# Kernel tuning notes

Hardware: AMD Instinct MI355X
Metric: run time of the kernel (lower is better)

## Reference

```python
import jax, jax.numpy as jnp
import numpy as np
import math

B, H, S, D = 2, 16, 2048, 64

def setup_inputs() -> dict:
    key = jax.random.key(0)
    kq, kk, kv, km = jax.random.split(key, 4)
    return {
        "query": jax.random.normal(kq, (B, H, S, D), dtype=jnp.float32),
        "key": jax.random.normal(kk, (B, H, S, D), dtype=jnp.float32),
        "value": jax.random.normal(kv, (B, H, S, D), dtype=jnp.float32),
        "mask": jax.random.randint(km, (B, 1, S, S), 0, 2, dtype=jnp.int32),
    }

def reference(query, key, value, mask):
    d = query.shape[-1]
    # scores: [B, H, S, S]
    scores = jnp.einsum("bhqd,bhkd->bhqk", query, key) / math.sqrt(d)
    masking_value = -1e9 if scores.dtype == jnp.float32 else -1e4
    scores = jnp.where(mask == 0, jnp.asarray(masking_value, scores.dtype), scores)
    p_attn = jax.nn.softmax(scores, axis=-1)
    out = jnp.einsum("bhqk,bhkd->bhqd", p_attn, value)
    return (out, p_attn)
```

## Files before the change

kernel.cpp:

```cpp
#include <hip/hip_runtime.h>

#define B_ 2
#define H_ 16
#define S_ 2048
#define D_ 64

typedef short v8s __attribute__((ext_vector_type(8)));
typedef float v4f __attribute__((ext_vector_type(4)));
typedef unsigned short u16;
typedef unsigned int   u32;
typedef unsigned long long u64;

__device__ __forceinline__ u32 pk2(float a, float b) {
    u32 ua = __float_as_uint(a) + 0x8000u;
    u32 ub = __float_as_uint(b) + 0x8000u;
    return __builtin_amdgcn_perm(ub, ua, 0x07060302u);
}

__device__ __forceinline__ v8s cvt8(const float* __restrict__ p, float s) {
    float4 x = ((const float4*)p)[0];
    float4 y = ((const float4*)p)[1];
    union { u32 u[4]; v8s v; } r;
    r.u[0] = pk2(x.x * s, x.y * s);
    r.u[1] = pk2(x.z * s, x.w * s);
    r.u[2] = pk2(y.x * s, y.y * s);
    r.u[3] = pk2(y.z * s, y.w * s);
    return r.v;
}

__device__ __forceinline__ void gll16(const void* g, void* l) {
    __builtin_amdgcn_global_load_lds(
        (const __attribute__((address_space(1))) u32*)g,
        (__attribute__((address_space(3))) u32*)l, 16, 0, 0);
}


__global__ void cvt_bf16_k(const float* __restrict__ src, u16* __restrict__ dst) {
    size_t i = (size_t)blockIdx.x * blockDim.x + threadIdx.x;
    const float* p = src + i * 8;
    float4 a = ((const float4*)p)[0], b = ((const float4*)p)[1];
    uint4 o;
    o.x = pk2(a.x, a.y); o.y = pk2(a.z, a.w);
    o.z = pk2(b.x, b.y); o.w = pk2(b.z, b.w);
    ((uint4*)dst)[i] = o;
}

__global__ void vtrans_k(const float* __restrict__ V, u16* __restrict__ Vt) {
    __shared__ u16 t[64][66];
    const int bh = blockIdx.y, s0 = blockIdx.x * 64;
    const int tid = threadIdx.x;
    {
        const int r = tid >> 2, c0 = (tid & 3) * 16;
        const float* p = V + ((size_t)bh * S_ + s0 + r) * D_ + c0;
        float4 f0 = ((const float4*)p)[0], f1 = ((const float4*)p)[1];
        float4 f2 = ((const float4*)p)[2], f3 = ((const float4*)p)[3];
        u32* tw = (u32*)&t[r][c0];
        tw[0] = pk2(f0.x, f0.y); tw[1] = pk2(f0.z, f0.w);
        tw[2] = pk2(f1.x, f1.y); tw[3] = pk2(f1.z, f1.w);
        tw[4] = pk2(f2.x, f2.y); tw[5] = pk2(f2.z, f2.w);
        tw[6] = pk2(f3.x, f3.y); tw[7] = pk2(f3.z, f3.w);
    }
    __syncthreads();
    {
        const int d = tid >> 2, t2 = tid & 3;
        const int G = t2 >> 1, hh = t2 & 1;
        const int e0 = G * 32 + hh * 8;
        u32 o[8];
        #pragma unroll
        for (int u = 0; u < 8; ++u)
            o[u] = (u32)t[e0 + u][d] | ((u32)t[e0 + 16 + u][d] << 16);
        u16* q = Vt + ((size_t)bh * D_ + d) * S_ + s0 + G * 32 + hh * 16;
        ((uint4*)q)[0] = make_uint4(o[0], o[1], o[2], o[3]);
        ((uint4*)q)[1] = make_uint4(o[4], o[5], o[6], o[7]);
    }
}

__global__ void mbits_k(const int* __restrict__ mask, u64* __restrict__ mb) {
    size_t i = (size_t)blockIdx.x * blockDim.x + threadIdx.x;
    u64 bal = __ballot(mask[i] != 0);
    if ((threadIdx.x & 63) == 0) mb[i >> 6] = bal;
}

__global__ __launch_bounds__(256, 4)
void attn_fast(const float* __restrict__ Q, const u16* __restrict__ Kb,
               const u16* __restrict__ Vt, const u32* __restrict__ mbits,
               float* __restrict__ out, float* __restrict__ P)
{
    __shared__ __align__(16) char LS[32768];

    const int tid = threadIdx.x;
    const int w = tid >> 6, lane = tid & 63;
    const int n = lane & 15, g = lane >> 4;

    const int x = blockIdx.x;
    const int xcd = x & 7, kk = x >> 3;
    const int bh = xcd * 4 + (kk >> 5);
    const int qb = kk & 31;
    const int b = bh >> 4;
    const int q0 = qb * 64 + w * 16;

    const float* qrow = Q + ((size_t)bh * S_ + q0 + n) * D_;
    const v8s aq0 = cvt8(qrow + g * 8, 0.125f);
    const v8s aq1 = cvt8(qrow + 32 + g * 8, 0.125f);

    const int srow = 16 * w + (lane >> 3);
    const int swz16 = (((lane & 7) ^ (srow & 7)) << 4);
    const char* kB  = (const char*)(Kb + (size_t)bh * S_ * D_) + (size_t)srow * 128 + swz16;
    const char* vB  = (const char*)(Vt + (size_t)bh * D_ * S_) + (size_t)srow * 4096 + swz16;
    const char* kBA = (const char*)(Kb + (size_t)bh * S_ * D_)
                      + (size_t)(32 * w + (lane >> 3)) * 128 + swz16;

    const int C = n * 128 + (((g) ^ (n & 7)) << 4);

    const u32* mroww = mbits + ((size_t)b * S_ + q0 + n) * 64;

    float sum = 0.f;
    {
        #pragma unroll
        for (int c = 0; c < 4; ++c)
            gll16(kBA + c * 1024, LS + (size_t)w * 4096 + c * 1024);
        uint4 mnx = *(const uint4*)(mroww);
        __syncthreads();

        for (int T = 0; T < 16; ++T) {
            const char* KA = LS + (T & 1) * 16384;
            if (T < 15) {
                const char* src = kBA + (size_t)(T + 1) * 16384;
                char* dst = LS + ((T + 1) & 1) * 16384 + (size_t)w * 4096;
                #pragma unroll
                for (int c = 0; c < 4; ++c) gll16(src + c * 1024, dst + c * 1024);
            }
            uint4 mc = mnx;
            if (T < 15) mnx = *(const uint4*)(mroww + (T + 1) * 4);

            v4f acc[8];
            __builtin_amdgcn_s_setprio(1);
            #pragma unroll
            for (int s = 0; s < 8; ++s) {
                v8s kf0 = *(const v8s*)(KA + s * 2048 + C);
                v8s kf1 = *(const v8s*)(KA + s * 2048 + (C ^ 64));
                v4f z = {0.f, 0.f, 0.f, 0.f};
                z = __builtin_amdgcn_mfma_f32_16x16x32_bf16(kf0, aq0, z, 0, 0, 0);
                acc[s] = __builtin_amdgcn_mfma_f32_16x16x32_bf16(kf1, aq1, z, 0, 0, 0);
            }
            __builtin_amdgcn_s_setprio(0);
            float ps0 = 0.f, ps1 = 0.f;
            #pragma unroll
            for (int s = 0; s < 8; ++s) {
                u32 wrd = (s >> 1) == 0 ? mc.x : (s >> 1) == 1 ? mc.y
                        : (s >> 1) == 2 ? mc.z : mc.w;
                #pragma unroll
                for (int i = 0; i < 4; ++i) {
                    float e = ((wrd >> ((s & 1) * 16 + 4 * g + i)) & 1)
                              ? __expf(acc[s][i]) : 0.f;
                    if (s & 1) ps1 += e; else ps0 += e;
                }
            }
            sum += ps0 + ps1;
            __syncthreads();
        }
    }
    sum += __shfl_xor(sum, 16, 64);
    sum += __shfl_xor(sum, 32, 64);
    const float inv = 1.0f / sum;

    float* pbB = P + ((size_t)bh * S_ + q0 + n) * S_;
    v4f o0 = {0.f, 0.f, 0.f, 0.f}, o1 = o0, o2 = o0, o3 = o0;
    {
        #pragma unroll
        for (int c = 0; c < 2; ++c) {
            gll16(kB + (size_t)c * 1024,  LS + (size_t)w * 2048 + c * 1024);
            gll16(vB + (size_t)c * 32768, LS + 8192 + (size_t)w * 2048 + c * 1024);
        }
        uint2 mnx = *(const uint2*)(mroww);
        __syncthreads();

        for (int t = 0; t < 32; ++t) {
            const char* Kc = LS + (t & 1) * 16384;
            const char* Vc = Kc + 8192;
            if (t < 31) {
                char* dstb = LS + ((t + 1) & 1) * 16384;
                const char* ks = kB + (size_t)(t + 1) * 8192;
                const char* vs = vB + (size_t)(t + 1) * 128;
                #pragma unroll
                for (int c = 0; c < 2; ++c) {
                    gll16(ks + (size_t)c * 1024,  dstb + (size_t)w * 2048 + c * 1024);
                    gll16(vs + (size_t)c * 32768, dstb + 8192 + (size_t)w * 2048 + c * 1024);
                }
            }
            uint2 mc = mnx;
            if (t < 31) mnx = *(const uint2*)(mroww + (t + 1) * 2);

            v4f a[4];
            __builtin_amdgcn_s_setprio(1);
            #pragma unroll
            for (int s = 0; s < 4; ++s) {
                v8s kf0 = *(const v8s*)(Kc + s * 2048 + C);
                v8s kf1 = *(const v8s*)(Kc + s * 2048 + (C ^ 64));
                v4f z = {0.f, 0.f, 0.f, 0.f};
                z = __builtin_amdgcn_mfma_f32_16x16x32_bf16(kf0, aq0, z, 0, 0, 0);
                a[s] = __builtin_amdgcn_mfma_f32_16x16x32_bf16(kf1, aq1, z, 0, 0, 0);
            }
            __builtin_amdgcn_s_setprio(0);

            float* pt = pbB + (size_t)t * 64;
            #pragma unroll
            for (int kg = 0; kg < 2; ++kg) {
                u32 wrd = kg ? mc.y : mc.x;
                v4f p0, p1;
                #pragma unroll
                for (int i = 0; i < 4; ++i) {
                    p0[i] = ((wrd >> (4 * g + i)) & 1)
                            ? __expf(a[2 * kg][i]) * inv : 0.f;
                    p1[i] = ((wrd >> (16 + 4 * g + i)) & 1)
                            ? __expf(a[2 * kg + 1][i]) * inv : 0.f;
                }
                __builtin_nontemporal_store(p0, (v4f*)(pt + kg * 32 + 4 * g));
                __builtin_nontemporal_store(p1, (v4f*)(pt + kg * 32 + 16 + 4 * g));
                union { u32 u[4]; v8s v; } ap;
                #pragma unroll
                for (int i = 0; i < 4; ++i) ap.u[i] = pk2(p0[i], p1[i]);
                __builtin_amdgcn_s_setprio(1);
                v8s vf0 = *(const v8s*)(Vc + 0 * 2048 + (C ^ (kg << 6)));
                v8s vf1 = *(const v8s*)(Vc + 1 * 2048 + (C ^ (kg << 6)));
                v8s vf2 = *(const v8s*)(Vc + 2 * 2048 + (C ^ (kg << 6)));
                v8s vf3 = *(const v8s*)(Vc + 3 * 2048 + (C ^ (kg << 6)));
                o0 = __builtin_amdgcn_mfma_f32_16x16x32_bf16(ap.v, vf0, o0, 0, 0, 0);
                o1 = __builtin_amdgcn_mfma_f32_16x16x32_bf16(ap.v, vf1, o1, 0, 0, 0);
                o2 = __builtin_amdgcn_mfma_f32_16x16x32_bf16(ap.v, vf2, o2, 0, 0, 0);
                o3 = __builtin_amdgcn_mfma_f32_16x16x32_bf16(ap.v, vf3, o3, 0, 0, 0);
                __builtin_amdgcn_s_setprio(0);
            }
            __syncthreads();
        }
    }

    float* obase = out + ((size_t)bh * S_ + q0 + 4 * g) * D_ + n;
    #pragma unroll
    for (int i = 0; i < 4; ++i) {
        __builtin_nontemporal_store(o0[i], obase + (size_t)i * D_);
        __builtin_nontemporal_store(o1[i], obase + (size_t)i * D_ + 16);
        __builtin_nontemporal_store(o2[i], obase + (size_t)i * D_ + 32);
        __builtin_nontemporal_store(o3[i], obase + (size_t)i * D_ + 48);
    }
}

__global__ __launch_bounds__(256, 4)
void attn_fb(const float* __restrict__ Q, const float* __restrict__ K,
             const float* __restrict__ V, const int* __restrict__ mask,
             float* __restrict__ out, float* __restrict__ P)
{
    __shared__ u16 ldsbuf[4][640];
    const int tid = threadIdx.x;
    const int w = tid >> 6, lane = tid & 63;
    const int n = lane & 15, g = lane >> 4;
    const int qb = blockIdx.x, h = blockIdx.y, b = blockIdx.z;
    const int bh = b * H_ + h;
    const int q0 = qb * 64 + w * 16;

    const float* qrow = Q + ((size_t)bh * S_ + q0 + n) * D_;
    const v8s aq0 = cvt8(qrow + g * 8, 0.125f);
    const v8s aq1 = cvt8(qrow + 32 + g * 8, 0.125f);

    const int* mrow = mask + ((size_t)b * S_ + q0 + g * 4) * S_ + n;
    const float* kfbase = K + ((size_t)bh * S_ + n) * D_ + g * 8;

    auto loadK = [&](int key0, int dh) -> v8s {
        return cvt8(kfbase + (size_t)key0 * D_ + dh * 32, 1.0f);
    };
    auto loadM = [&](int i, int k0) -> u32 {
        u32 r = 0;
        if (mrow[(size_t)i * S_ + k0]) r |= 1u << n;
        if (mrow[(size_t)i * S_ + k0 + 16]) r |= 1u << (n + 16);
        return r;
    };
    auto loadV = [&](int k0, int dt) -> v8s {
        union { u32 u[4]; v8s v; } r;
        const float* vp = V + ((size_t)bh * S_ + k0 + g * 4) * D_ + dt * 16 + n;
        #pragma unroll
        for (int p2 = 0; p2 < 4; ++p2) {
            float fa = vp[(size_t)p2 * D_];
            float fb = vp[(size_t)(16 + p2) * D_];
            r.u[p2] = pk2(fa, fb);
        }
        return r.v;
    };

    v4f sum = {0.f, 0.f, 0.f, 0.f};
    for (int k0 = 0; k0 < S_; k0 += 32) {
        v4f a0 = {0.f, 0.f, 0.f, 0.f}, a1 = {0.f, 0.f, 0.f, 0.f};
        a0 = __builtin_amdgcn_mfma_f32_16x16x32_bf16(aq0, loadK(k0, 0), a0, 0, 0, 0);
        a0 = __builtin_amdgcn_mfma_f32_16x16x32_bf16(aq1, loadK(k0, 1), a0, 0, 0, 0);
        a1 = __builtin_amdgcn_mfma_f32_16x16x32_bf16(aq0, loadK(k0 + 16, 0), a1, 0, 0, 0);
        a1 = __builtin_amdgcn_mfma_f32_16x16x32_bf16(aq1, loadK(k0 + 16, 1), a1, 0, 0, 0);
        #pragma unroll
        for (int i = 0; i < 4; ++i) {
            u32 mw = loadM(i, k0);
            float e0 = ((mw >> n) & 1) ? __expf(a0[i]) : 0.f;
            float e1 = ((mw >> (n + 16)) & 1) ? __expf(a1[i]) : 0.f;
            sum[i] += e0 + e1;
        }
    }
    #pragma unroll
    for (int i = 0; i < 4; ++i) {
        float s = sum[i];
        s += __shfl_xor(s, 1, 64);
        s += __shfl_xor(s, 2, 64);
        s += __shfl_xor(s, 4, 64);
        s += __shfl_xor(s, 8, 64);
        sum[i] = 1.0f / s;
    }

    char* ldsw = (char*)&ldsbuf[w][0];
    float* pbase = P + ((size_t)bh * S_ + q0 + g * 4) * S_ + n;
    v4f o0 = {0.f, 0.f, 0.f, 0.f}, o1 = o0, o2 = o0, o3 = o0;

    for (int k0 = 0; k0 < S_; k0 += 32) {
        v4f a0 = {0.f, 0.f, 0.f, 0.f}, a1 = {0.f, 0.f, 0.f, 0.f};
        a0 = __builtin_amdgcn_mfma_f32_16x16x32_bf16(aq0, loadK(k0, 0), a0, 0, 0, 0);
        a0 = __builtin_amdgcn_mfma_f32_16x16x32_bf16(aq1, loadK(k0, 1), a0, 0, 0, 0);
        a1 = __builtin_amdgcn_mfma_f32_16x16x32_bf16(aq0, loadK(k0 + 16, 0), a1, 0, 0, 0);
        a1 = __builtin_amdgcn_mfma_f32_16x16x32_bf16(aq1, loadK(k0 + 16, 1), a1, 0, 0, 0);
        #pragma unroll
        for (int i = 0; i < 4; ++i) {
            u32 mw = loadM(i, k0);
            float p0 = ((mw >> n) & 1) ? __expf(a0[i]) * sum[i] : 0.f;
            float p1 = ((mw >> (n + 16)) & 1) ? __expf(a1[i]) * sum[i] : 0.f;
            pbase[(size_t)i * S_ + k0] = p0;
            pbase[(size_t)i * S_ + k0 + 16] = p1;
            *(u32*)(ldsw + (g * 4 + i) * 80 + (n >> 2) * 16 + (n & 3) * 4) = pk2(p0, p1);
        }
        v8s ap = *(const v8s*)(ldsw + n * 80 + g * 16);
        o0 = __builtin_amdgcn_mfma_f32_16x16x32_bf16(ap, loadV(k0, 0), o0, 0, 0, 0);
        o1 = __builtin_amdgcn_mfma_f32_16x16x32_bf16(ap, loadV(k0, 1), o1, 0, 0, 0);
        o2 = __builtin_amdgcn_mfma_f32_16x16x32_bf16(ap, loadV(k0, 2), o2, 0, 0, 0);
        o3 = __builtin_amdgcn_mfma_f32_16x16x32_bf16(ap, loadV(k0, 3), o3, 0, 0, 0);
    }

    float* obase = out + ((size_t)bh * S_ + q0 + g * 4) * D_ + n;
    #pragma unroll
    for (int i = 0; i < 4; ++i) {
        obase[(size_t)i * D_]      = o0[i];
        obase[(size_t)i * D_ + 16] = o1[i];
        obase[(size_t)i * D_ + 32] = o2[i];
        obase[(size_t)i * D_ + 48] = o3[i];
    }
}

extern "C" void kernel_launch(void* const* d_in, const int* in_sizes, int n_in,
                              void* d_out, int out_size, void* d_ws, size_t ws_size,
                              hipStream_t stream)
{
    (void)in_sizes; (void)n_in; (void)out_size;
    const float* Q = (const float*)d_in[0];
    const float* K = (const float*)d_in[1];
    const float* V = (const float*)d_in[2];
    const int* mask = (const int*)d_in[3];
    float* out = (float*)d_out;
    float* P = out + (size_t)B_ * H_ * S_ * D_;

    const size_t kb_b = (size_t)B_ * H_ * S_ * D_ * 2;
    const size_t vt_b = kb_b;
    const size_t mb_b = (size_t)B_ * S_ * S_ / 8;

    if (ws_size >= kb_b + vt_b + mb_b) {
        u16* Kb = (u16*)d_ws;
        u16* Vt = (u16*)((char*)d_ws + kb_b);
        u64* mb = (u64*)((char*)d_ws + kb_b + vt_b);
        cvt_bf16_k<<<(B_ * H_ * S_ * D_) / (256 * 8), 256, 0, stream>>>(K, Kb);
        vtrans_k<<<dim3(S_ / 64, B_ * H_), 256, 0, stream>>>(V, Vt);
        mbits_k<<<(B_ * S_ * S_) / 256, 256, 0, stream>>>(mask, mb);
        attn_fast<<<B_ * H_ * (S_ / 64), 256, 0, stream>>>(Q, Kb, Vt, (const u32*)mb, out, P);
    } else {
        attn_fb<<<dim3(S_ / 64, H_, B_), 256, 0, stream>>>(Q, K, V, mask, out, P);
    }
}
```

Before: 687.5 us.

## Load K/V MFMA fragments directly from global memory into registers, dropping LDS staging

```diff
diff --git a/kernel.cpp b/kernel.cpp
--- a/kernel.cpp
+++ b/kernel.cpp
@@ -26,12 +26,6 @@
     r.u[2] = pk2(y.x * s, y.y * s);
     r.u[3] = pk2(y.z * s, y.w * s);
     return r.v;
-}
-
-__device__ __forceinline__ void gll16(const void* g, void* l) {
-    __builtin_amdgcn_global_load_lds(
-        (const __attribute__((address_space(1))) u32*)g,
-        (__attribute__((address_space(3))) u32*)l, 16, 0, 0);
 }
 
 
@@ -86,8 +80,6 @@
                const u16* __restrict__ Vt, const u32* __restrict__ mbits,
                float* __restrict__ out, float* __restrict__ P)
 {
-    __shared__ __align__(16) char LS[32768];
-
     const int tid = threadIdx.x;
     const int w = tid >> 6, lane = tid & 63;
     const int n = lane & 15, g = lane >> 4;
@@ -103,62 +95,54 @@
     const v8s aq0 = cvt8(qrow + g * 8, 0.125f);
     const v8s aq1 = cvt8(qrow + 32 + g * 8, 0.125f);
 
-    const int srow = 16 * w + (lane >> 3);
-    const int swz16 = (((lane & 7) ^ (srow & 7)) << 4);
-    const char* kB  = (const char*)(Kb + (size_t)bh * S_ * D_) + (size_t)srow * 128 + swz16;
-    const char* vB  = (const char*)(Vt + (size_t)bh * D_ * S_) + (size_t)srow * 4096 + swz16;
-    const char* kBA = (const char*)(Kb + (size_t)bh * S_ * D_)
-                      + (size_t)(32 * w + (lane >> 3)) * 128 + swz16;
-
-    const int C = n * 128 + (((g) ^ (n & 7)) << 4);
-
+    const char* kfl = (const char*)Kb + (size_t)bh * S_ * D_ * 2 + n * 128 + g * 16;
+    const char* vfl = (const char*)Vt + (size_t)bh * D_ * S_ * 2 + n * 4096 + g * 16;
     const u32* mroww = mbits + ((size_t)b * S_ + q0 + n) * 64;
 
     float sum = 0.f;
+    struct KFrag { v8s h0[4]; v8s h1[4]; uint2 m; };
+    auto loadA = [&](KFrag& F, int T) {
+        const char* kp = kfl + (size_t)T * 64 * 128;
+        #pragma unroll
+        for (int s = 0; s < 4; ++s) {
+            F.h0[s] = *(const v8s*)(kp + s * 16 * 128);
+            F.h1[s] = *(const v8s*)(kp + s * 16 * 128 + 64);
+        }
+        F.m = *(const uint2*)(mroww + T * 2);
+    };
+    auto compA = [&](const KFrag& F) {
+        v4f acc[4];
+        __builtin_amdgcn_s_setprio(1);
+        #pragma unroll
+        for (int s = 0; s < 4; ++s) {
+            v4f z = {0.f, 0.f, 0.f, 0.f};
+            z = __builtin_amdgcn_mfma_f32_16x16x32_bf16(F.h0[s], aq0, z, 0, 0, 0);
+            acc[s] = __builtin_amdgcn_mfma_f32_16x16x32_bf16(F.h1[s], aq1, z, 0, 0, 0);
+        }
+        __builtin_amdgcn_s_setprio(0);
+        #pragma unroll
+        for (int s = 0; s < 4; ++s) {
+            u32 wrd = (s >> 1) ? F.m.y : F.m.x;
+            #pragma unroll
+            for (int i = 0; i < 4; ++i) {
+                float e = ((wrd >> ((s & 1) * 16 + 4 * g + i)) & 1)
+                          ? __expf(acc[s][i]) : 0.f;
+                sum += e;
+            }
+        }
+    };
     {
-        #pragma unroll
-        for (int c = 0; c < 4; ++c)
-            gll16(kBA + c * 1024, LS + (size_t)w * 4096 + c * 1024);
-        uint4 mnx = *(const uint4*)(mroww);
-        __syncthreads();
-
-        for (int T = 0; T < 16; ++T) {
-            const char* KA = LS + (T & 1) * 16384;
-            if (T < 15) {
-                const char* src = kBA + (size_t)(T + 1) * 16384;
-                char* dst = LS + ((T + 1) & 1) * 16384 + (size_t)w * 4096;
-                #pragma unroll
-                for (int c = 0; c < 4; ++c) gll16(src + c * 1024, dst + c * 1024);
-            }
-            uint4 mc = mnx;
-            if (T < 15) mnx = *(const uint4*)(mroww + (T + 1) * 4);
-
-            v4f acc[8];
-            __builtin_amdgcn_s_setprio(1);
-            #pragma unroll
-            for (int s = 0; s < 8; ++s) {
-                v8s kf0 = *(const v8s*)(KA + s * 2048 + C);
-                v8s kf1 = *(const v8s*)(KA + s * 2048 + (C ^ 64));
-                v4f z = {0.f, 0.f, 0.f, 0.f};
-                z = __builtin_amdgcn_mfma_f32_16x16x32_bf16(kf0, aq0, z, 0, 0, 0);
-                acc[s] = __builtin_amdgcn_mfma_f32_16x16x32_bf16(kf1, aq1, z, 0, 0, 0);
-            }
-            __builtin_amdgcn_s_setprio(0);
-            float ps0 = 0.f, ps1 = 0.f;
-            #pragma unroll
-            for (int s = 0; s < 8; ++s) {
-                u32 wrd = (s >> 1) == 0 ? mc.x : (s >> 1) == 1 ? mc.y
-                        : (s >> 1) == 2 ? mc.z : mc.w;
-                #pragma unroll
-                for (int i = 0; i < 4; ++i) {
-                    float e = ((wrd >> ((s & 1) * 16 + 4 * g + i)) & 1)
-                              ? __expf(acc[s][i]) : 0.f;
-                    if (s & 1) ps1 += e; else ps0 += e;
-                }
-            }
-            sum += ps0 + ps1;
-            __syncthreads();
-        }
+        KFrag fa, fb2;
+        loadA(fa, 0);
+        for (int T = 0; T < 30; T += 2) {
+            loadA(fb2, T + 1);
+            compA(fa);
+            loadA(fa, T + 2);
+            compA(fb2);
+        }
+        loadA(fb2, 31);
+        compA(fa);
+        compA(fb2);
     }
     sum += __shfl_xor(sum, 16, 64);
     sum += __shfl_xor(sum, 32, 64);
@@ -166,73 +150,64 @@
 
     float* pbB = P + ((size_t)bh * S_ + q0 + n) * S_;
     v4f o0 = {0.f, 0.f, 0.f, 0.f}, o1 = o0, o2 = o0, o3 = o0;
+
+    struct BFrag { v8s k00, k01, k10, k11; v8s v[4]; u32 m; };
+    auto loadB = [&](BFrag& F, int j) {
+        const char* kp = kfl + (size_t)j * 32 * 128;
+        F.k00 = *(const v8s*)(kp);
+        F.k01 = *(const v8s*)(kp + 64);
+        F.k10 = *(const v8s*)(kp + 16 * 128);
+        F.k11 = *(const v8s*)(kp + 16 * 128 + 64);
+        const char* vp = vfl + (size_t)j * 64;
+        #pragma unroll
+        for (int dt = 0; dt < 4; ++dt)
+            F.v[dt] = *(const v8s*)(vp + (size_t)dt * 65536);
+        F.m = mroww[j];
+    };
+    auto compB = [&](const BFrag& F, int j) {
+        v4f a0, a1;
+        __builtin_amdgcn_s_setprio(1);
+        {
+            v4f z = {0.f, 0.f, 0.f, 0.f};
+            z = __builtin_amdgcn_mfma_f32_16x16x32_bf16(F.k00, aq0, z, 0, 0, 0);
+            a0 = __builtin_amdgcn_mfma_f32_16x16x32_bf16(F.k01, aq1, z, 0, 0, 0);
+        }
+        {
+            v4f z = {0.f, 0.f, 0.f, 0.f};
+            z = __builtin_amdgcn_mfma_f32_16x16x32_bf16(F.k10, aq0, z, 0, 0, 0);
+            a1 = __builtin_amdgcn_mfma_f32_16x16x32_bf16(F.k11, aq1, z, 0, 0, 0);
+        }
+        __builtin_amdgcn_s_setprio(0);
+        v4f p0, p1;
+        #pragma unroll
+        for (int i = 0; i < 4; ++i) {
+            p0[i] = ((F.m >> (4 * g + i)) & 1)      ? __expf(a0[i]) * inv : 0.f;
+            p1[i] = ((F.m >> (16 + 4 * g + i)) & 1) ? __expf(a1[i]) * inv : 0.f;
+        }
+        __builtin_nontemporal_store(p0, (v4f*)(pbB + j * 32 + 4 * g));
+        __builtin_nontemporal_store(p1, (v4f*)(pbB + j * 32 + 16 + 4 * g));
+        union { u32 u[4]; v8s v; } ap;
+        #pragma unroll
+        for (int i = 0; i < 4; ++i) ap.u[i] = pk2(p0[i], p1[i]);
+        __builtin_amdgcn_s_setprio(1);
+        o0 = __builtin_amdgcn_mfma_f32_16x16x32_bf16(ap.v, F.v[0], o0, 0, 0, 0);
+        o1 = __builtin_amdgcn_mfma_f32_16x16x32_bf16(ap.v, F.v[1], o1, 0, 0, 0);
+        o2 = __builtin_amdgcn_mfma_f32_16x16x32_bf16(ap.v, F.v[2], o2, 0, 0, 0);
+        o3 = __builtin_amdgcn_mfma_f32_16x16x32_bf16(ap.v, F.v[3], o3, 0, 0, 0);
+        __builtin_amdgcn_s_setprio(0);
+    };
     {
-        #pragma unroll
-        for (int c = 0; c < 2; ++c) {
-            gll16(kB + (size_t)c * 1024,  LS + (size_t)w * 2048 + c * 1024);
-            gll16(vB + (size_t)c * 32768, LS + 8192 + (size_t)w * 2048 + c * 1024);
-        }
-        uint2 mnx = *(const uint2*)(mroww);
-        __syncthreads();
-
-        for (int t = 0; t < 32; ++t) {
-            const char* Kc = LS + (t & 1) * 16384;
-            const char* Vc = Kc + 8192;
-            if (t < 31) {
-                char* dstb = LS + ((t + 1) & 1) * 16384;
-                const char* ks = kB + (size_t)(t + 1) * 8192;
-                const char* vs = vB + (size_t)(t + 1) * 128;
-                #pragma unroll
-                for (int c = 0; c < 2; ++c) {
-                    gll16(ks + (size_t)c * 1024,  dstb + (size_t)w * 2048 + c * 1024);
-                    gll16(vs + (size_t)c * 32768, dstb + 8192 + (size_t)w * 2048 + c * 1024);
-                }
-            }
-            uint2 mc = mnx;
-            if (t < 31) mnx = *(const uint2*)(mroww + (t + 1) * 2);
-
-            v4f a[4];
-            __builtin_amdgcn_s_setprio(1);
-            #pragma unroll
-            for (int s = 0; s < 4; ++s) {
-                v8s kf0 = *(const v8s*)(Kc + s * 2048 + C);
-                v8s kf1 = *(const v8s*)(Kc + s * 2048 + (C ^ 64));
-                v4f z = {0.f, 0.f, 0.f, 0.f};
-                z = __builtin_amdgcn_mfma_f32_16x16x32_bf16(kf0, aq0, z, 0, 0, 0);
-                a[s] = __builtin_amdgcn_mfma_f32_16x16x32_bf16(kf1, aq1, z, 0, 0, 0);
-            }
-            __builtin_amdgcn_s_setprio(0);
-
-            float* pt = pbB + (size_t)t * 64;
-            #pragma unroll
-            for (int kg = 0; kg < 2; ++kg) {
-                u32 wrd = kg ? mc.y : mc.x;
-                v4f p0, p1;
-                #pragma unroll
-                for (int i = 0; i < 4; ++i) {
-                    p0[i] = ((wrd >> (4 * g + i)) & 1)
-                            ? __expf(a[2 * kg][i]) * inv : 0.f;
-                    p1[i] = ((wrd >> (16 + 4 * g + i)) & 1)
-                            ? __expf(a[2 * kg + 1][i]) * inv : 0.f;
-                }
-                __builtin_nontemporal_store(p0, (v4f*)(pt + kg * 32 + 4 * g));
-                __builtin_nontemporal_store(p1, (v4f*)(pt + kg * 32 + 16 + 4 * g));
-                union { u32 u[4]; v8s v; } ap;
-                #pragma unroll
-                for (int i = 0; i < 4; ++i) ap.u[i] = pk2(p0[i], p1[i]);
-                __builtin_amdgcn_s_setprio(1);
-                v8s vf0 = *(const v8s*)(Vc + 0 * 2048 + (C ^ (kg << 6)));
-                v8s vf1 = *(const v8s*)(Vc + 1 * 2048 + (C ^ (kg << 6)));
-                v8s vf2 = *(const v8s*)(Vc + 2 * 2048 + (C ^ (kg << 6)));
-                v8s vf3 = *(const v8s*)(Vc + 3 * 2048 + (C ^ (kg << 6)));
-                o0 = __builtin_amdgcn_mfma_f32_16x16x32_bf16(ap.v, vf0, o0, 0, 0, 0);
-                o1 = __builtin_amdgcn_mfma_f32_16x16x32_bf16(ap.v, vf1, o1, 0, 0, 0);
-                o2 = __builtin_amdgcn_mfma_f32_16x16x32_bf16(ap.v, vf2, o2, 0, 0, 0);
-                o3 = __builtin_amdgcn_mfma_f32_16x16x32_bf16(ap.v, vf3, o3, 0, 0, 0);
-                __builtin_amdgcn_s_setprio(0);
-            }
-            __syncthreads();
-        }
+        BFrag ga, gb;
+        loadB(ga, 0);
+        for (int j = 0; j < 62; j += 2) {
+            loadB(gb, j + 1);
+            compB(ga, j);
+            loadB(ga, j + 2);
+            compB(gb, j + 1);
+        }
+        loadB(gb, 63);
+        compB(ga, 62);
+        compB(gb, 63);
     }
 
     float* obase = out + ((size_t)bh * S_ + q0 + 4 * g) * D_ + n;
```

Result: slower. 888.6 us (+29.2%).
